# Performance work log

Measured on AMD Instinct MI355X. Metric: run time of the kernel, lower is better.

The kernel has to match this reference:

```python
import jax, jax.numpy as jnp
import numpy as np

D_STATE = 16  # Mamba d_state for both blocks


def causal_conv(x, w, b):
    # x: [b, l, d]; w: [d, k] depthwise kernel; torch Conv1d(groups=d, padding=k-1)
    # then truncated to length l == causal left-padding of k-1.
    d, k = w.shape
    kern = w.T[:, None, :]  # [k, 1, d] for ('NLC','LIO','NLC')
    y = jax.lax.conv_general_dilated(x, kern, (1,), [(k - 1, 0)],
                                     dimension_numbers=('NLC', 'LIO', 'NLC'),
                                     feature_group_count=d)
    return y + b


def selective_scan(u, dt, A, Bm, Cm, D):
    # u, dt: [b,l,d]; A: [d,n]; Bm, Cm: [b,l,n]; D: [d]
    dA = jnp.exp(dt[..., None] * A)                               # [b,l,d,n]
    dBu = dt[..., None] * Bm[:, :, None, :] * u[..., None]        # [b,l,d,n]

    def step(h, inp):
        dA_t, dBu_t, C_t = inp
        h = dA_t * h + dBu_t                                      # [b,d,n]
        return h, jnp.einsum('bdn,bn->bd', h, C_t)

    h0 = jnp.zeros((u.shape[0],) + A.shape, u.dtype)
    _, ys = jax.lax.scan(step, h0, (jnp.swapaxes(dA, 0, 1),
                                    jnp.swapaxes(dBu, 0, 1),
                                    jnp.swapaxes(Cm, 0, 1)))
    return jnp.swapaxes(ys, 0, 1) + u * D


def mamba(x, in_w, conv_w, conv_b, xproj_w, dt_w, dt_b, A_log, D, out_w):
    # Reference (non-fused) Mamba block, mamba_simple semantics.
    dt_rank = dt_w.shape[0]
    xz = x @ in_w                                                 # [b,l,2*d_inner]
    xi, z = jnp.split(xz, 2, axis=-1)
    xi = jax.nn.silu(causal_conv(xi, conv_w, conv_b))
    x_dbl = xi @ xproj_w                                          # [b,l,dt_rank+2n]
    dt = jax.nn.softplus(x_dbl[..., :dt_rank] @ dt_w + dt_b)
    Bm = x_dbl[..., dt_rank:dt_rank + D_STATE]
    Cm = x_dbl[..., dt_rank + D_STATE:]
    y = selective_scan(xi, dt, -jnp.exp(A_log), Bm, Cm, D)
    return (y * jax.nn.silu(z)) @ out_w


def setup_inputs() -> dict:
    key = jax.random.key(0)
    ks = iter(jax.random.split(key, 32))
    B, K, N, DM = 8, 1024, 98, 2048

    def w(shape, s=0.02):
        return jax.random.normal(next(ks), shape, jnp.float32) * s

    a_Alog = jnp.log(jnp.tile(jnp.arange(1., 17., dtype=jnp.float32)[None, :], (196, 1)))
    c_Alog = jnp.log(jnp.tile(jnp.arange(1., 17., dtype=jnp.float32)[None, :], (4096, 1)))
    return dict(
        imageFeature=jax.random.normal(next(ks), (N, DM), jnp.float32),
        kf=jax.random.normal(next(ks), (B, DM, K), jnp.float32),
        # atten Mamba: d_model=98, d_inner=196, dt_rank=7
        a_in_w=w((98, 392)), a_conv_w=w((196, 4), 0.3), a_conv_b=jnp.zeros((196,), jnp.float32),
        a_xproj_w=w((196, 7 + 2 * D_STATE)), a_dt_w=w((7, 196)), a_dt_b=jnp.zeros((196,), jnp.float32),
        a_A_log=a_Alog, a_D=jnp.ones((196,), jnp.float32), a_out_w=w((196, 98)),
        # cross Mamba: d_model=2048, d_inner=4096, dt_rank=128
        c_in_w=w((2048, 8192)), c_conv_w=w((4096, 4), 0.3), c_conv_b=jnp.zeros((4096,), jnp.float32),
        c_xproj_w=w((4096, 128 + 2 * D_STATE)), c_dt_w=w((128, 4096)), c_dt_b=jnp.zeros((4096,), jnp.float32),
        c_A_log=c_Alog, c_D=jnp.ones((4096,), jnp.float32), c_out_w=w((4096, 2048)),
    )


def reference(imageFeature, kf, a_in_w, a_conv_w, a_conv_b, a_xproj_w, a_dt_w, a_dt_b,
              a_A_log, a_D, a_out_w, c_in_w, c_conv_w, c_conv_b, c_xproj_w, c_dt_w,
              c_dt_b, c_A_log, c_D, c_out_w):
    kf_t = jnp.swapaxes(kf, 1, 2)                                 # [B,K,2048]
    # IKScore = kf^T @ imageFeature^T : [B,K,98]
    score = jnp.einsum('bkd,nd->bkn', kf_t, imageFeature)
    score = mamba(score, a_in_w, a_conv_w, a_conv_b, a_xproj_w, a_dt_w, a_dt_b,
                  a_A_log, a_D, a_out_w)
    # AdaptiveAvgPool1d(1) over last dim, softmax over K
    s = jax.nn.softmax(score.mean(-1), axis=1)                    # [B,K]
    vtopk, ind = jax.lax.top_k(s, 98)                             # top-98 over K
    # fused batched gather + scale (replaces the per-batch Python loop)
    src = jnp.take_along_axis(kf_t, ind[:, :, None], axis=1) * vtopk[:, :, None]  # [B,98,2048]
    # cross Mamba with extra_emb: extra stream fused additively into hidden states
    h = imageFeature[None, :, :] + src                            # [B,98,2048]
    return mamba(h, c_in_w, c_conv_w, c_conv_b, c_xproj_w, c_dt_w,
                 c_dt_b, c_A_log, c_D, c_out_w)
```

## Files before the change

kernel.cpp:

```cpp
#include <hip/hip_runtime.h>
#include <hip/hip_bf16.h>
#include <math.h>

typedef __attribute__((ext_vector_type(8))) short short8;
typedef __attribute__((ext_vector_type(4))) float floatx4;

__device__ __forceinline__ float siluf(float x) {
    float e = __expf(-fabsf(x));
    float s = (x >= 0.f) ? 1.f / (1.f + e) : e / (1.f + e);
    return x * s;
}
__device__ __forceinline__ float softplusf(float x) {
    if (x > 20.f) return x;
    if (x < -20.f) return __expf(x);
    return log1pf(__expf(x));
}
__device__ __forceinline__ unsigned short f2b(float v) {
    __hip_bfloat16 b = __float2bfloat16(v);
    unsigned short u;
    __builtin_memcpy(&u, &b, 2);
    return u;
}
template<int CTRL>
__device__ __forceinline__ float dpp_add(float x) {
    int yi = __builtin_amdgcn_mov_dpp(__float_as_int(x), CTRL, 0xF, 0xF, true);
    return x + __int_as_float(yi);
}
__device__ __forceinline__ float row16_sum(float p) {
    p = dpp_add<0xB1>(p);
    p = dpp_add<0x4E>(p);
    p = dpp_add<0x124>(p);
    p = dpp_add<0x128>(p);
    return p;
}

template<bool ACOL, bool BCOL, bool AMUL, int EPI>
__global__ __launch_bounds__(256) void gemm64(
    const float* __restrict__ A, const float* __restrict__ Bw, float* __restrict__ C,
    const float* __restrict__ A2, const float* __restrict__ bias,
    int M, int N, int K, int lda, int ldb, int ldc, int lda2,
    long batA, long batB, long batC)
{
    __shared__ __align__(16) float As[16][68];
    __shared__ __align__(16) float Bs[16][68];
    int tx = threadIdx.x;
    int m0 = blockIdx.x * 64, n0 = blockIdx.y * 64;
    A += blockIdx.z * batA; Bw += blockIdx.z * batB; C += blockIdx.z * batC;
    int tm = tx >> 4, tn = tx & 15;
    float acc[4][4] = {};
    for (int k0 = 0; k0 < K; k0 += 16) {
        for (int i = tx; i < 1024; i += 256) {
            int mm, kk;
            if (ACOL) { mm = i & 63; kk = i >> 6; } else { kk = i & 15; mm = i >> 4; }
            int m = m0 + mm, k = k0 + kk;
            float v = 0.f;
            if (m < M && k < K) {
                long ia = ACOL ? ((long)k * lda + m) : ((long)m * lda + k);
                v = A[ia];
                if (AMUL) v *= siluf(A2[(long)m * lda2 + k]);
            }
            As[kk][mm] = v;
        }
        for (int i = tx; i < 1024; i += 256) {
            int nn, kk;
            if (BCOL) { kk = i & 15; nn = i >> 4; } else { nn = i & 63; kk = i >> 6; }
            int n = n0 + nn, k = k0 + kk;
            float v = 0.f;
            if (n < N && k < K) {
                long ib = BCOL ? ((long)n * ldb + k) : ((long)k * ldb + n);
                v = Bw[ib];
            }
            Bs[kk][nn] = v;
        }
        __syncthreads();
#pragma unroll
        for (int kk = 0; kk < 16; ++kk) {
            float4 av = *(const float4*)&As[kk][tm * 4];
            float4 bv = *(const float4*)&Bs[kk][tn * 4];
            float a[4] = {av.x, av.y, av.z, av.w};
            float b[4] = {bv.x, bv.y, bv.z, bv.w};
#pragma unroll
            for (int i = 0; i < 4; i++)
#pragma unroll
                for (int j = 0; j < 4; j++) acc[i][j] += a[i] * b[j];
        }
        __syncthreads();
    }
#pragma unroll
    for (int i = 0; i < 4; i++) {
        int m = m0 + tm * 4 + i;
        if (m >= M) continue;
#pragma unroll
        for (int j = 0; j < 4; j++) {
            int n = n0 + tn * 4 + j;
            if (n >= N) continue;
            float v = acc[i][j];
            if (EPI == 1) v = softplusf(v + bias[n]);
            C[(long)m * ldc + n] = v;
        }
    }
}

__global__ __launch_bounds__(256) void gemm64_sk(
    const float* __restrict__ A, const float* __restrict__ Bw, float* __restrict__ Cpart,
    int M, int N, int K, int lda, int ldb, int kch)
{
    __shared__ __align__(16) float As[16][68];
    __shared__ __align__(16) float Bs[16][68];
    int tx = threadIdx.x;
    int m0 = blockIdx.x * 64, n0 = blockIdx.y * 64;
    int kbeg = blockIdx.z * kch;
    int kend = min(kbeg + kch, K);
    Cpart += (long)blockIdx.z * M * N;
    int tm = tx >> 4, tn = tx & 15;
    float acc[4][4] = {};
    for (int k0 = kbeg; k0 < kend; k0 += 16) {
        for (int i = tx; i < 1024; i += 256) {
            int kk = i & 15, mm = i >> 4;
            int m = m0 + mm, k = k0 + kk;
            As[kk][mm] = (m < M && k < kend) ? A[(long)m * lda + k] : 0.f;
        }
        for (int i = tx; i < 1024; i += 256) {
            int nn = i & 63, kk = i >> 6;
            int n = n0 + nn, k = k0 + kk;
            Bs[kk][nn] = (n < N && k < kend) ? Bw[(long)k * ldb + n] : 0.f;
        }
        __syncthreads();
#pragma unroll
        for (int kk = 0; kk < 16; ++kk) {
            float4 av = *(const float4*)&As[kk][tm * 4];
            float4 bv = *(const float4*)&Bs[kk][tn * 4];
            float a[4] = {av.x, av.y, av.z, av.w};
            float b[4] = {bv.x, bv.y, bv.z, bv.w};
#pragma unroll
            for (int i = 0; i < 4; i++)
#pragma unroll
                for (int j = 0; j < 4; j++) acc[i][j] += a[i] * b[j];
        }
        __syncthreads();
    }
#pragma unroll
    for (int i = 0; i < 4; i++) {
        int m = m0 + tm * 4 + i;
        if (m >= M) continue;
#pragma unroll
        for (int j = 0; j < 4; j++) {
            int n = n0 + tn * 4 + j;
            if (n >= N) continue;
            Cpart[(long)m * N + n] = acc[i][j];
        }
    }
}

__global__ __launch_bounds__(256) void gemm_s1(
    const float* __restrict__ kf, const float* __restrict__ img,
    float* __restrict__ Cpart)
{
    __shared__ __align__(16) float As[16][68];
    __shared__ __align__(16) float Bs[16][68];
    int tx = threadIdx.x;
    int m0 = blockIdx.x * 64, n0 = blockIdx.y * 64;
    int bz = blockIdx.z >> 3, kz = blockIdx.z & 7;
    const float* A = kf + (long)bz * 2048 * 1024;
    float* Cp = Cpart + (long)kz * 802816 + (long)bz * 100352;
    int kbeg = kz * 256;
    int tm = tx >> 4, tn = tx & 15;
    int akk = tx >> 4, amq = (tx & 15) * 4;
    int bnn = tx >> 2, bkq = (tx & 3) * 4;
    bool bvalid = (n0 + bnn) < 98;
    const float* Bp = img + (long)(n0 + bnn) * 2048;
    float acc[4][4] = {};
    for (int k0 = kbeg; k0 < kbeg + 256; k0 += 16) {
        float4 av = *(const float4*)&A[(long)(k0 + akk) * 1024 + m0 + amq];
        float4 bv = bvalid ? *(const float4*)&Bp[k0 + bkq] : (float4){0.f, 0.f, 0.f, 0.f};
        __syncthreads();
        *(float4*)&As[akk][amq] = av;
        Bs[bkq + 0][bnn] = bv.x;
        Bs[bkq + 1][bnn] = bv.y;
        Bs[bkq + 2][bnn] = bv.z;
        Bs[bkq + 3][bnn] = bv.w;
        __syncthreads();
#pragma unroll
        for (int kk = 0; kk < 16; ++kk) {
            float4 a4 = *(const float4*)&As[kk][tm * 4];
            float4 b4 = *(const float4*)&Bs[kk][tn * 4];
            float a[4] = {a4.x, a4.y, a4.z, a4.w};
            float b[4] = {b4.x, b4.y, b4.z, b4.w};
#pragma unroll
            for (int i = 0; i < 4; i++)
#pragma unroll
                for (int j = 0; j < 4; j++) acc[i][j] += a[i] * b[j];
        }
    }
#pragma unroll
    for (int i = 0; i < 4; i++) {
        int m = m0 + tm * 4 + i;
#pragma unroll
        for (int j = 0; j < 4; j++) {
            int n = n0 + tn * 4 + j;
            if (n < 98) Cp[(long)m * 98 + n] = acc[i][j];
        }
    }
}

__global__ void sk_reduce(const float* __restrict__ Cpart, float* __restrict__ C,
                          long len, int nz)
{
    long i = (long)blockIdx.x * 256 + threadIdx.x;
    if (i >= len) return;
    float s = 0.f;
    for (int z = 0; z < nz; z++) s += Cpart[(long)z * len + i];
    C[i] = s;
}

__global__ __launch_bounds__(256) void mfma_gemm(
    const unsigned short* __restrict__ Abf, const unsigned short* __restrict__ Bbf,
    float* __restrict__ C, int M, int N, int K, int ldc)
{
    __shared__ __align__(16) short As[128 * 40];
    __shared__ __align__(16) short Bs[128 * 40];
    int tid = threadIdx.x;
    int m0 = blockIdx.x * 128, n0 = blockIdx.y * 128;
    int w = tid >> 6, l = tid & 63;
    int wm = (w >> 1) * 64, wn = (w & 1) * 64;
    int lr = l & 15, lq = l >> 4;
    int row0 = tid >> 2, kc = (tid & 3) * 8;
    floatx4 acc[4][4];
#pragma unroll
    for (int i = 0; i < 4; i++)
#pragma unroll
        for (int j = 0; j < 4; j++) acc[i][j] = (floatx4){0.f, 0.f, 0.f, 0.f};
    const unsigned short* Ap  = Abf + (long)(m0 + row0) * K + kc;
    const unsigned short* Ap2 = Abf + (long)(m0 + row0 + 64) * K + kc;
    const unsigned short* Bp  = Bbf + (long)(n0 + row0) * K + kc;
    const unsigned short* Bp2 = Bbf + (long)(n0 + row0 + 64) * K + kc;
    for (int k0 = 0; k0 < K; k0 += 32) {
        uint4 a0 = *(const uint4*)(Ap + k0);
        uint4 a1 = *(const uint4*)(Ap2 + k0);
        uint4 b0 = *(const uint4*)(Bp + k0);
        uint4 b1 = *(const uint4*)(Bp2 + k0);
        __syncthreads();
        *(uint4*)&As[row0 * 40 + kc] = a0;
        *(uint4*)&As[(row0 + 64) * 40 + kc] = a1;
        *(uint4*)&Bs[row0 * 40 + kc] = b0;
        *(uint4*)&Bs[(row0 + 64) * 40 + kc] = b1;
        __syncthreads();
        short8 af[4], bfr[4];
#pragma unroll
        for (int i = 0; i < 4; i++) af[i]  = *(const short8*)&As[(wm + i * 16 + lr) * 40 + lq * 8];
#pragma unroll
        for (int i = 0; i < 4; i++) bfr[i] = *(const short8*)&Bs[(wn + i * 16 + lr) * 40 + lq * 8];
#pragma unroll
        for (int i = 0; i < 4; i++)
#pragma unroll
            for (int j = 0; j < 4; j++)
                acc[i][j] = __builtin_amdgcn_mfma_f32_16x16x32_bf16(af[i], bfr[j], acc[i][j], 0, 0, 0);
    }
#pragma unroll
    for (int i = 0; i < 4; i++) {
#pragma unroll
        for (int r = 0; r < 4; r++) {
            int m = m0 + wm + i * 16 + lq * 4 + r;
            if (m >= M) continue;
#pragma unroll
            for (int j = 0; j < 4; j++)
                C[(long)m * ldc + n0 + wn + j * 16 + lr] = acc[i][j][r];
        }
    }
}

__global__ __launch_bounds__(256) void tpose_cvt(const float* __restrict__ src,
                                                 unsigned short* __restrict__ dst,
                                                 int K, int N)
{
    __shared__ float t[32][33];
    int n0 = blockIdx.x * 32, k0 = blockIdx.y * 32;
    int tid = threadIdx.x;
    int r = tid >> 3, c4 = (tid & 7) * 4;
    float4 v = *(const float4*)&src[(long)(k0 + r) * N + n0 + c4];
    t[r][c4] = v.x; t[r][c4 + 1] = v.y; t[r][c4 + 2] = v.z; t[r][c4 + 3] = v.w;
    __syncthreads();
    ushort4 o;
    o.x = f2b(t[c4][r]);
    o.y = f2b(t[c4 + 1][r]);
    o.z = f2b(t[c4 + 2][r]);
    o.w = f2b(t[c4 + 3][r]);
    *(ushort4*)&dst[(long)(n0 + r) * K + k0 + c4] = o;
}

__global__ void cvt_pad(const float* __restrict__ src, unsigned short* __restrict__ dst,
                        int M, int Mpad, int C)
{
    long i4 = ((long)blockIdx.x * 256 + threadIdx.x) * 4;
    if (i4 >= (long)Mpad * C) return;
    int row = (int)(i4 / C);
    ushort4 o = {0, 0, 0, 0};
    if (row < M) {
        float4 v = *(const float4*)&src[i4];
        o.x = f2b(v.x); o.y = f2b(v.y); o.z = f2b(v.z); o.w = f2b(v.w);
    }
    *(ushort4*)&dst[i4] = o;
}

__global__ void gate_cvt(const float* __restrict__ y, const float* __restrict__ z,
                         unsigned short* __restrict__ dst, int M, int Mpad, int C, int ldz)
{
    long i4 = ((long)blockIdx.x * 256 + threadIdx.x) * 4;
    if (i4 >= (long)Mpad * C) return;
    int row = (int)(i4 / C);
    int col = (int)(i4 - (long)row * C);
    ushort4 o = {0, 0, 0, 0};
    if (row < M) {
        float4 yv = *(const float4*)&y[i4];
        float4 zv = *(const float4*)&z[(long)row * ldz + col];
        o.x = f2b(yv.x * siluf(zv.x));
        o.y = f2b(yv.y * siluf(zv.y));
        o.z = f2b(yv.z * siluf(zv.z));
        o.w = f2b(yv.w * siluf(zv.w));
    }
    *(ushort4*)&dst[i4] = o;
}

__global__ void conv_silu_kernel(const float* __restrict__ xz, const float* __restrict__ w,
                                 const float* __restrict__ bias, float* __restrict__ out,
                                 int Bn, int L, int din, int ldx)
{
    int idx = blockIdx.x * 256 + threadIdx.x;
    int total = Bn * L * din;
    if (idx >= total) return;
    int c = idx % din;
    int r = idx / din;
    int t = r % L;
    int b = r / L;
    float acc = bias[c];
#pragma unroll
    for (int i = 0; i < 4; i++) {
        int tt = t - 3 + i;
        if (tt >= 0) acc += w[c * 4 + i] * xz[((long)(b * L + tt)) * ldx + c];
    }
    out[idx] = siluf(acc);
}

template<int T>
__global__ __launch_bounds__(256) void scan_kernel(
    const float* u, const float* dt,
    const float* xdbl, const float* __restrict__ A_log,
    const float* __restrict__ Dp, float* y,
    int din, int L, int xld, int boff, int coff)
{
    constexpr int ST = ((T - 4 + 31) / 32) * 32 + 4;
    __shared__ __align__(16) float dtc[16][ST], uc[16][ST];
    __shared__ __align__(16) float Bc[16][ST], Cc[16][ST], yc[16][ST];
    int tx = threadIdx.x;
    int dl = tx >> 4;
    int n = tx & 15;
    int dbase = blockIdx.x * 16;
    int dg = dbase + dl;
    int b = blockIdx.y;
    bool act = dg < din;
    float Acoef = act ? -__expf(A_log[dg * 16 + n]) : 0.f;
    float Dv = act ? Dp[dg] : 0.f;
    int nvalid = min(16, din - dbase);
    float h = 0.f;
    for (int c0 = 0; c0 < L; c0 += T) {
        int tcnt = min(T, L - c0);
        for (int i = tx; i < T * 16; i += 256) {
            int tt = i >> 4, c = i & 15;
            if (tt < tcnt) {
                long row = (long)b * L + c0 + tt;
                float uv = 0.f, dv = 0.f;
                if (c < nvalid) { uv = u[row * din + dbase + c]; dv = dt[row * din + dbase + c]; }
                uc[c][tt] = uv; dtc[c][tt] = dv;
                Bc[c][tt] = xdbl[row * xld + boff + c];
                Cc[c][tt] = xdbl[row * xld + coff + c];
            }
        }
        __syncthreads();
        int tt = 0;
        for (; tt + 16 <= tcnt; tt += 16) {
            float4 dt4[4], u4[4], B4[4], C4[4];
#pragma unroll
            for (int g = 0; g < 4; g++) {
                dt4[g] = *(const float4*)&dtc[dl][tt + g * 4];
                u4[g]  = *(const float4*)&uc[dl][tt + g * 4];
                B4[g]  = *(const float4*)&Bc[n][tt + g * 4];
                C4[g]  = *(const float4*)&Cc[n][tt + g * 4];
            }
            float pbuf[16];
#pragma unroll
            for (int g = 0; g < 4; g++) {
                float dts[4] = {dt4[g].x, dt4[g].y, dt4[g].z, dt4[g].w};
                float us[4]  = {u4[g].x, u4[g].y, u4[g].z, u4[g].w};
                float bs[4]  = {B4[g].x, B4[g].y, B4[g].z, B4[g].w};
                float cs[4]  = {C4[g].x, C4[g].y, C4[g].z, C4[g].w};
#pragma unroll
                for (int s = 0; s < 4; s++) {
                    float dA = __expf(dts[s] * Acoef);
                    h = dA * h + (dts[s] * us[s]) * bs[s];
                    pbuf[g * 4 + s] = h * cs[s];
                }
            }
#pragma unroll
            for (int q = 0; q < 16; q++) pbuf[q] = row16_sum(pbuf[q]);
            if (n == 0) {
#pragma unroll
                for (int g = 0; g < 4; g++) {
                    float4 y4;
                    y4.x = pbuf[g * 4 + 0] + Dv * u4[g].x;
                    y4.y = pbuf[g * 4 + 1] + Dv * u4[g].y;
                    y4.z = pbuf[g * 4 + 2] + Dv * u4[g].z;
                    y4.w = pbuf[g * 4 + 3] + Dv * u4[g].w;
                    *(float4*)&yc[dl][tt + g * 4] = y4;
                }
            }
        }
        for (; tt < tcnt; ++tt) {
            float dtv = dtc[dl][tt];
            float uv  = uc[dl][tt];
            float dA = __expf(dtv * Acoef);
            h = dA * h + (dtv * uv) * Bc[n][tt];
            float p = row16_sum(h * Cc[n][tt]);
            if (n == 0) yc[dl][tt] = p + Dv * uv;
        }
        __syncthreads();
        for (int i = tx; i < tcnt * 16; i += 256) {
            int tt2 = i >> 4, c = i & 15;
            if (c < nvalid) y[((long)b * L + c0 + tt2) * din + dbase + c] = yc[c][tt2];
        }
        __syncthreads();
    }
}

__global__ __launch_bounds__(256) void row_mean_kernel(const float* __restrict__ sc2,
                                                       float* __restrict__ means)
{
    int row = blockIdx.x * 4 + (threadIdx.x >> 6);
    int lane = threadIdx.x & 63;
    const float* p = sc2 + (long)row * 98;
    float s = p[lane];
    if (lane < 34) s += p[lane + 64];
    s += __shfl_xor(s, 1);
    s += __shfl_xor(s, 2);
    s += __shfl_xor(s, 4);
    s += __shfl_xor(s, 8);
    s += __shfl_xor(s, 16);
    s += __shfl_xor(s, 32);
    if (lane == 0) means[row] = s * (1.f / 98.f);
}

__global__ __launch_bounds__(256) void softmax1024_kernel(const float* __restrict__ means,
                                                          float* __restrict__ s)
{
    __shared__ float red[256];
    int b = blockIdx.x, tx = threadIdx.x;
    float v[4];
    float mx = -1e30f;
#pragma unroll
    for (int i = 0; i < 4; i++) {
        v[i] = means[b * 1024 + tx + i * 256];
        mx = fmaxf(mx, v[i]);
    }
    red[tx] = mx; __syncthreads();
    for (int st = 128; st > 0; st >>= 1) { if (tx < st) red[tx] = fmaxf(red[tx], red[tx + st]); __syncthreads(); }
    mx = red[0]; __syncthreads();
    float lsum = 0.f;
#pragma unroll
    for (int i = 0; i < 4; i++) { v[i] = __expf(v[i] - mx); lsum += v[i]; }
    red[tx] = lsum; __syncthreads();
    for (int st = 128; st > 0; st >>= 1) { if (tx < st) red[tx] += red[tx + st]; __syncthreads(); }
    float inv = 1.f / red[0];
#pragma unroll
    for (int i = 0; i < 4; i++) s[b * 1024 + tx + i * 256] = v[i] * inv;
}

__global__ __launch_bounds__(256) void topk_select_kernel(const float* __restrict__ s,
                                                          int* __restrict__ ind,
                                                          float* __restrict__ vtopk)
{
    __shared__ unsigned long long arr[1024];
    __shared__ unsigned long long red[256];
    int b = blockIdx.x, tx = threadIdx.x;
    for (int k = tx; k < 1024; k += 256) {
        float v = s[b * 1024 + k];
        unsigned u = __float_as_uint(v);
        u = (u & 0x80000000u) ? ~u : (u | 0x80000000u);
        arr[k] = ((unsigned long long)u << 32) | (unsigned)(~k);
    }
    __syncthreads();
    for (int r = 0; r < 98; ++r) {
        unsigned long long m = 0ull;
        for (int k = tx; k < 1024; k += 256) m = (arr[k] > m) ? arr[k] : m;
        red[tx] = m; __syncthreads();
        for (int st = 128; st > 0; st >>= 1) {
            if (tx < st && red[tx + st] > red[tx]) red[tx] = red[tx + st];
            __syncthreads();
        }
        unsigned long long best = red[0];
        if (tx == 0) {
            unsigned lo = (unsigned)(best & 0xffffffffu);
            int kidx = (int)(~lo);
            unsigned ub = (unsigned)(best >> 32);
            unsigned fb = (ub & 0x80000000u) ? (ub ^ 0x80000000u) : ~ub;
            ind[b * 98 + r] = kidx;
            vtopk[b * 98 + r] = __uint_as_float(fb);
            arr[kidx] = 0ull;
        }
        __syncthreads();
    }
}

__global__ void gather_kernel(const float* __restrict__ img, const float* __restrict__ kf,
                              const int* __restrict__ ind, const float* __restrict__ vtopk,
                              float* __restrict__ h)
{
    int j = blockIdx.x, b = blockIdx.y;
    int kidx = ind[b * 98 + j];
    float v = vtopk[b * 98 + j];
    long hbase = ((long)b * 98 + j) * 2048;
    const float* kfb = kf + (long)b * 2048 * 1024 + kidx;
    for (int d = threadIdx.x; d < 2048; d += 256)
        h[hbase + d] = img[(long)j * 2048 + d] + kfb[(long)d * 1024] * v;
}

extern "C" void kernel_launch(void* const* d_in, const int* in_sizes, int n_in,
                              void* d_out, int out_size, void* d_ws, size_t ws_size,
                              hipStream_t stream)
{
    const float* imgF      = (const float*)d_in[0];
    const float* kf        = (const float*)d_in[1];
    const float* a_in_w    = (const float*)d_in[2];
    const float* a_conv_w  = (const float*)d_in[3];
    const float* a_conv_b  = (const float*)d_in[4];
    const float* a_xproj_w = (const float*)d_in[5];
    const float* a_dt_w    = (const float*)d_in[6];
    const float* a_dt_b    = (const float*)d_in[7];
    const float* a_A_log   = (const float*)d_in[8];
    const float* a_D       = (const float*)d_in[9];
    const float* a_out_w   = (const float*)d_in[10];
    const float* c_in_w    = (const float*)d_in[11];
    const float* c_conv_w  = (const float*)d_in[12];
    const float* c_conv_b  = (const float*)d_in[13];
    const float* c_xproj_w = (const float*)d_in[14];
    const float* c_dt_w    = (const float*)d_in[15];
    const float* c_dt_b    = (const float*)d_in[16];
    const float* c_A_log   = (const float*)d_in[17];
    const float* c_D       = (const float*)d_in[18];
    const float* c_out_w   = (const float*)d_in[19];

    float* fout = (float*)d_out;

    float* ws = (float*)d_ws;
    float* h_buf  = ws;
    float* S      = ws + 1605632;
    float* score  = S;
    float* xz_a   = S + 802816;
    float* xi_a   = S + 4014080;
    float* xdbl_a = S + 5619712;
    float* dt_a   = S + 5939200;
    float* sbuf   = S + 7544832;
    int*   indb   = (int*)(S + 7553024);
    float* vtopk  = S + 7553808;
    float* xz_c   = S;
    float* xi_c   = S + 6422528;
    float* xdbl_c = S + 9633792;
    float* dt_c   = S + 9759232;
    unsigned short* cwbf  = (unsigned short*)(ws + 14576128);
    unsigned short* h_bf  = (unsigned short*)(ws + 14576128 + 8388608);
    unsigned short* yz_bf = (unsigned short*)(ws + 14576128 + 9306112);
    float* CpartS1 = ws + 14576128;
    float* Cpart  = ws + 18770432;
    float* means  = dt_a;

    gemm_s1<<<dim3(16, 2, 64), 256, 0, stream>>>(kf, imgF, CpartS1);
    sk_reduce<<<3136, 256, 0, stream>>>(CpartS1, score, 802816L, 8);

    gemm64<false, false, false, 0><<<dim3(128, 7, 1), 256, 0, stream>>>(
        score, a_in_w, xz_a, nullptr, nullptr, 8192, 392, 98, 98, 392, 392, 0, 0L, 0L, 0L);
    conv_silu_kernel<<<6272, 256, 0, stream>>>(xz_a, a_conv_w, a_conv_b, xi_a, 8, 1024, 196, 392);
    gemm64<false, false, false, 0><<<dim3(128, 1, 1), 256, 0, stream>>>(
        xi_a, a_xproj_w, xdbl_a, nullptr, nullptr, 8192, 39, 196, 196, 39, 39, 0, 0L, 0L, 0L);
    gemm64<false, false, false, 1><<<dim3(128, 4, 1), 256, 0, stream>>>(
        xdbl_a, a_dt_w, dt_a, nullptr, a_dt_b, 8192, 196, 7, 39, 196, 196, 0, 0L, 0L, 0L);
    scan_kernel<64><<<dim3(13, 8, 1), 256, 0, stream>>>(
        xi_a, dt_a, xdbl_a, a_A_log, a_D, xi_a, 196, 1024, 39, 7, 23);
    gemm64<false, false, true, 0><<<dim3(128, 2, 1), 256, 0, stream>>>(
        xi_a, a_out_w, score, xz_a + 196, nullptr, 8192, 98, 196, 196, 98, 98, 392, 0L, 0L, 0L);
    row_mean_kernel<<<2048, 256, 0, stream>>>(score, means);
    softmax1024_kernel<<<8, 256, 0, stream>>>(means, sbuf);
    topk_select_kernel<<<8, 256, 0, stream>>>(sbuf, indb, vtopk);
    gather_kernel<<<dim3(98, 8, 1), 256, 0, stream>>>(imgF, kf, indb, vtopk, h_buf);

    tpose_cvt<<<dim3(256, 64, 1), 256, 0, stream>>>(c_in_w, cwbf, 2048, 8192);
    cvt_pad<<<1792, 256, 0, stream>>>(h_buf, h_bf, 784, 896, 2048);
    mfma_gemm<<<dim3(7, 64, 1), 256, 0, stream>>>(h_bf, cwbf, xz_c, 784, 8192, 2048, 8192);

    conv_silu_kernel<<<12544, 256, 0, stream>>>(xz_c, c_conv_w, c_conv_b, xi_c, 8, 98, 4096, 8192);

    gemm64_sk<<<dim3(13, 3, 16), 256, 0, stream>>>(
        xi_c, c_xproj_w, Cpart, 784, 160, 4096, 4096, 160, 256);
    sk_reduce<<<490, 256, 0, stream>>>(Cpart, xdbl_c, 125440L, 16);

    gemm64<false, false, false, 1><<<dim3(13, 64, 1), 256, 0, stream>>>(
        xdbl_c, c_dt_w, dt_c, nullptr, c_dt_b, 784, 4096, 128, 160, 4096, 4096, 0, 0L, 0L, 0L);

    scan_kernel<98><<<dim3(256, 8, 1), 256, 0, stream>>>(
        xi_c, dt_c, xdbl_c, c_A_log, c_D, xi_c, 4096, 98, 160, 128, 144);

    gate_cvt<<<3584, 256, 0, stream>>>(xi_c, xz_c + 4096, yz_bf, 784, 896, 4096, 8192);
    tpose_cvt<<<dim3(64, 128, 1), 256, 0, stream>>>(c_out_w, cwbf, 4096, 2048);
    mfma_gemm<<<dim3(7, 16, 1), 256, 0, stream>>>(yz_bf, cwbf, fout, 784, 2048, 4096, 2048);
}
```

Before: 935.8 us.

## Split-K the output MFMA GEMM and register-prefetch next K tile

```diff
diff --git a/kernel.cpp b/kernel.cpp
--- a/kernel.cpp
+++ b/kernel.cpp
@@ -215,12 +215,15 @@
 
 __global__ __launch_bounds__(256) void mfma_gemm(
     const unsigned short* __restrict__ Abf, const unsigned short* __restrict__ Bbf,
-    float* __restrict__ C, int M, int N, int K, int ldc)
+    float* __restrict__ Cp, int M, int N, int K, int ldc, int kch, long partStride)
 {
     __shared__ __align__(16) short As[128 * 40];
     __shared__ __align__(16) short Bs[128 * 40];
     int tid = threadIdx.x;
     int m0 = blockIdx.x * 128, n0 = blockIdx.y * 128;
+    int kbeg = blockIdx.z * kch;
+    int kend = kbeg + kch;
+    float* C = Cp + (long)blockIdx.z * partStride;
     int w = tid >> 6, l = tid & 63;
     int wm = (w >> 1) * 64, wn = (w & 1) * 64;
     int lr = l & 15, lq = l >> 4;
@@ -234,16 +237,23 @@
     const unsigned short* Ap2 = Abf + (long)(m0 + row0 + 64) * K + kc;
     const unsigned short* Bp  = Bbf + (long)(n0 + row0) * K + kc;
     const unsigned short* Bp2 = Bbf + (long)(n0 + row0 + 64) * K + kc;
-    for (int k0 = 0; k0 < K; k0 += 32) {
-        uint4 a0 = *(const uint4*)(Ap + k0);
-        uint4 a1 = *(const uint4*)(Ap2 + k0);
-        uint4 b0 = *(const uint4*)(Bp + k0);
-        uint4 b1 = *(const uint4*)(Bp2 + k0);
+    uint4 a0 = *(const uint4*)(Ap + kbeg);
+    uint4 a1 = *(const uint4*)(Ap2 + kbeg);
+    uint4 b0 = *(const uint4*)(Bp + kbeg);
+    uint4 b1 = *(const uint4*)(Bp2 + kbeg);
+    for (int k0 = kbeg; k0 < kend; k0 += 32) {
         __syncthreads();
         *(uint4*)&As[row0 * 40 + kc] = a0;
         *(uint4*)&As[(row0 + 64) * 40 + kc] = a1;
         *(uint4*)&Bs[row0 * 40 + kc] = b0;
         *(uint4*)&Bs[(row0 + 64) * 40 + kc] = b1;
+        int kn = k0 + 32;
+        if (kn < kend) {
+            a0 = *(const uint4*)(Ap + kn);
+            a1 = *(const uint4*)(Ap2 + kn);
+            b0 = *(const uint4*)(Bp + kn);
+            b1 = *(const uint4*)(Bp2 + kn);
+        }
         __syncthreads();
         short8 af[4], bfr[4];
 #pragma unroll
@@ -570,6 +580,7 @@
     float* CpartS1 = ws + 14576128;
     float* Cpart  = ws + 18770432;
     float* means  = dt_a;
+    float* Cpart16 = S;
 
     gemm_s1<<<dim3(16, 2, 64), 256, 0, stream>>>(kf, imgF, CpartS1);
     sk_reduce<<<3136, 256, 0, stream>>>(CpartS1, score, 802816L, 8);
@@ -592,7 +603,8 @@
 
     tpose_cvt<<<dim3(256, 64, 1), 256, 0, stream>>>(c_in_w, cwbf, 2048, 8192);
     cvt_pad<<<1792, 256, 0, stream>>>(h_buf, h_bf, 784, 896, 2048);
-    mfma_gemm<<<dim3(7, 64, 1), 256, 0, stream>>>(h_bf, cwbf, xz_c, 784, 8192, 2048, 8192);
+    mfma_gemm<<<dim3(7, 64, 1), 256, 0, stream>>>(
+        h_bf, cwbf, xz_c, 784, 8192, 2048, 8192, 2048, 0L);
 
     conv_silu_kernel<<<12544, 256, 0, stream>>>(xz_c, c_conv_w, c_conv_b, xi_c, 8, 98, 4096, 8192);
 
@@ -608,5 +620,7 @@
 
     gate_cvt<<<3584, 256, 0, stream>>>(xi_c, xz_c + 4096, yz_bf, 784, 896, 4096, 8192);
     tpose_cvt<<<dim3(64, 128, 1), 256, 0, stream>>>(c_out_w, cwbf, 4096, 2048);
-    mfma_gemm<<<dim3(7, 16, 1), 256, 0, stream>>>(yz_bf, cwbf, fout, 784, 2048, 4096, 2048);
-}
+    mfma_gemm<<<dim3(7, 16, 4), 256, 0, stream>>>(
+        yz_bf, cwbf, Cpart16, 784, 2048, 4096, 2048, 1024, 1605632L);
+    sk_reduce<<<6272, 256, 0, stream>>>(Cpart16, fout, 1605632L, 4);
+}
```

After: 855.9 us. -8.5%, faster.
